# Kernel tuning notes

Measured on AMD Instinct MI355X. Metric: run time of the kernel, lower is better.

The kernel has to match this reference:

```python
import jax, jax.numpy as jnp
import numpy as np

# RReLU in eval mode is leaky_relu with slope = (lower+upper)/2 = (1/8 + 1/3)/2
RRELU_SLOPE = (1.0 / 8.0 + 1.0 / 3.0) / 2.0  # = 11/48

N_NODES, FEAT_DIM = 100000, 512
EMBED_DIM = 256
BATCH, NUM_SAMPLE = 16384, 10


def setup_inputs() -> dict:
    key = jax.random.key(0)
    k1, k2, k3 = jax.random.split(key, 3)
    features = jax.random.normal(k1, (N_NODES, FEAT_DIM), dtype=jnp.float32)
    # Xavier-uniform-style init for the weight [embed_dim, feat_dim]
    bound = float(np.sqrt(6.0 / (EMBED_DIM + FEAT_DIM)))
    weight = jax.random.uniform(k2, (EMBED_DIM, FEAT_DIM), dtype=jnp.float32,
                                minval=-bound, maxval=bound)
    # Pre-sampled neighbor ids per batch node: [BATCH, NUM_SAMPLE]
    neigh_idx = jax.random.randint(k3, (BATCH, NUM_SAMPLE), 0, N_NODES, dtype=jnp.int64)
    return {"features": features, "weight": weight, "neigh_idx": neigh_idx}


def reference(features, weight, neigh_idx):
    # Mean aggregator: gather sampled neighbor features and average -> [B, F]
    agg = jnp.take(features, neigh_idx, axis=0).mean(axis=1)
    # weight.mm(agg.t()) -> [E, B]
    y = jnp.einsum("ef,bf->eb", weight, agg)
    # RReLU (eval mode): leaky with mean slope
    return jnp.where(y >= 0, y, y * RRELU_SLOPE)
```

## Files before the change

### kernel.cpp

```cpp
#include <hip/hip_runtime.h>
#include <stdint.h>

constexpr int FEAT  = 512;
constexpr int EMB   = 256;
constexpr int BATCH = 16384;
constexpr int NSAMP = 10;
constexpr int NB    = 64;
constexpr float SLOPE  = 11.0f / 48.0f;
constexpr float INV_NS = 1.0f / 10.0f;

using f32x4 = __attribute__((ext_vector_type(4))) float;
using frag8 = __attribute__((ext_vector_type(8))) short;

static __device__ __forceinline__ unsigned f2b(float x) {
    unsigned u = __builtin_bit_cast(unsigned, x);
    return (u + 0x7fffu + ((u >> 16) & 1u)) >> 16;
}
static __device__ __forceinline__ unsigned pk2(float lo, float hi) {
    return f2b(lo) | (f2b(hi) << 16);
}

__global__ __launch_bounds__(512, 2) void enc_fused(const float* __restrict__ feat,
                                                    const float* __restrict__ wgt,
                                                    const int*   __restrict__ idx,
                                                    float*       __restrict__ out) {
    __shared__ ushort Bs[NB * FEAT];

    const int tid  = threadIdx.x;
    const int wv   = tid >> 6;
    const int lane = tid & 63;
    const int n0   = blockIdx.x * NB;

#pragma unroll 2
    for (int rr = 0; rr < 8; ++rr) {
        const int r  = wv * 8 + rr;
        const int ru = __builtin_amdgcn_readfirstlane(r);
        const int* ib = idx + (size_t)(n0 + ru) * NSAMP;
        f32x4 s0 = {0.f, 0.f, 0.f, 0.f}, s1 = {0.f, 0.f, 0.f, 0.f};
#pragma unroll
        for (int j = 0; j < NSAMP; ++j) {
            const float* fp = feat + (size_t)ib[j] * FEAT + lane * 8;
            const f32x4 v0 = *reinterpret_cast<const f32x4*>(fp);
            const f32x4 v1 = *reinterpret_cast<const f32x4*>(fp + 4);
            s0 += v0; s1 += v1;
        }
        union { frag8 f; unsigned u[4]; } o;
        o.u[0] = pk2(s0[0] * INV_NS, s0[1] * INV_NS);
        o.u[1] = pk2(s0[2] * INV_NS, s0[3] * INV_NS);
        o.u[2] = pk2(s1[0] * INV_NS, s1[1] * INV_NS);
        o.u[3] = pk2(s1[2] * INV_NS, s1[3] * INV_NS);
        const int kb = (lane * 16) ^ ((r & 7) << 4);
        *reinterpret_cast<frag8*>((char*)Bs + r * (FEAT * 2) + kb) = o.f;
    }
    __syncthreads();

    const int l15 = lane & 15, lq = lane >> 4;
    const int m0w = wv * 32;

    f32x4 acc[2][4] = {};

#pragma unroll
    for (int k0 = 0; k0 < FEAT; k0 += 32) {
        frag8 af[2], bf[4];
#pragma unroll
        for (int i = 0; i < 2; ++i) {
            const float* wp = wgt + (size_t)(m0w + i * 16 + l15) * FEAT + k0 + lq * 8;
            const f32x4 a0 = *reinterpret_cast<const f32x4*>(wp);
            const f32x4 a1 = *reinterpret_cast<const f32x4*>(wp + 4);
            union { frag8 f; unsigned u[4]; } pk;
            pk.u[0] = pk2(a0[0], a0[1]);
            pk.u[1] = pk2(a0[2], a0[3]);
            pk.u[2] = pk2(a1[0], a1[1]);
            pk.u[3] = pk2(a1[2], a1[3]);
            af[i] = pk.f;
        }
#pragma unroll
        for (int j = 0; j < 4; ++j) {
            const int row = j * 16 + l15;
            const int kb  = (k0 * 2 + lq * 16) ^ ((row & 7) << 4);
            bf[j] = *reinterpret_cast<const frag8*>((const char*)Bs + row * (FEAT * 2) + kb);
        }
#pragma unroll
        for (int i = 0; i < 2; ++i)
#pragma unroll
            for (int j = 0; j < 4; ++j)
                acc[i][j] = __builtin_amdgcn_mfma_f32_16x16x32_bf16(af[i], bf[j], acc[i][j], 0, 0, 0);
    }

#pragma unroll
    for (int i = 0; i < 2; ++i) {
        const int rb = m0w + i * 16 + lq * 4;
#pragma unroll
        for (int j = 0; j < 4; ++j) {
            const int col = n0 + j * 16 + l15;
#pragma unroll
            for (int q = 0; q < 4; ++q) {
                float y = acc[i][j][q];
                y = (y >= 0.f) ? y : y * SLOPE;
                out[(size_t)(rb + q) * BATCH + col] = y;
            }
        }
    }
}

extern "C" void kernel_launch(void* const* d_in, const int* in_sizes, int n_in,
                              void* d_out, int out_size, void* d_ws, size_t ws_size,
                              hipStream_t stream) {
    const float* feat = (const float*)d_in[0];
    const float* wgt  = (const float*)d_in[1];
    const int*   idx  = (const int*)d_in[2];
    float*       out  = (float*)d_out;

    enc_fused<<<BATCH / NB, 512, 0, stream>>>(feat, wgt, idx, out);
}
```

Measured before the change: 68.19 us.

## Use 1024-thread blocks with 16 waves, each owning a 16-row output strip

```diff
diff --git a/kernel.cpp b/kernel.cpp
--- a/kernel.cpp
+++ b/kernel.cpp
@@ -1,4 +1,5 @@
 #include <hip/hip_runtime.h>
+#include <hip/hip_bf16.h>
 #include <stdint.h>
 
 constexpr int FEAT  = 512;
@@ -6,24 +7,24 @@
 constexpr int BATCH = 16384;
 constexpr int NSAMP = 10;
 constexpr int NB    = 64;
+constexpr int NW    = 16;
+constexpr int RPW   = NB / NW;
 constexpr float SLOPE  = 11.0f / 48.0f;
 constexpr float INV_NS = 1.0f / 10.0f;
 
 using f32x4 = __attribute__((ext_vector_type(4))) float;
 using frag8 = __attribute__((ext_vector_type(8))) short;
 
-static __device__ __forceinline__ unsigned f2b(float x) {
-    unsigned u = __builtin_bit_cast(unsigned, x);
-    return (u + 0x7fffu + ((u >> 16) & 1u)) >> 16;
-}
-static __device__ __forceinline__ unsigned pk2(float lo, float hi) {
-    return f2b(lo) | (f2b(hi) << 16);
+static __device__ __forceinline__ unsigned bpack2(float a, float b) {
+    __hip_bfloat162 h = __float22bfloat162_rn(make_float2(a, b));
+    unsigned u; __builtin_memcpy(&u, &h, 4);
+    return u;
 }
 
-__global__ __launch_bounds__(512, 2) void enc_fused(const float* __restrict__ feat,
-                                                    const float* __restrict__ wgt,
-                                                    const int*   __restrict__ idx,
-                                                    float*       __restrict__ out) {
+__global__ __launch_bounds__(1024, 4) void enc_fused(const float* __restrict__ feat,
+                                                     const float* __restrict__ wgt,
+                                                     const int*   __restrict__ idx,
+                                                     float*       __restrict__ out) {
     __shared__ ushort Bs[NB * FEAT];
 
     const int tid  = threadIdx.x;
@@ -32,8 +33,8 @@
     const int n0   = blockIdx.x * NB;
 
 #pragma unroll 2
-    for (int rr = 0; rr < 8; ++rr) {
-        const int r  = wv * 8 + rr;
+    for (int rr = 0; rr < RPW; ++rr) {
+        const int r  = wv * RPW + rr;
         const int ru = __builtin_amdgcn_readfirstlane(r);
         const int* ib = idx + (size_t)(n0 + ru) * NSAMP;
         f32x4 s0 = {0.f, 0.f, 0.f, 0.f}, s1 = {0.f, 0.f, 0.f, 0.f};
@@ -45,60 +46,52 @@
             s0 += v0; s1 += v1;
         }
         union { frag8 f; unsigned u[4]; } o;
-        o.u[0] = pk2(s0[0] * INV_NS, s0[1] * INV_NS);
-        o.u[1] = pk2(s0[2] * INV_NS, s0[3] * INV_NS);
-        o.u[2] = pk2(s1[0] * INV_NS, s1[1] * INV_NS);
-        o.u[3] = pk2(s1[2] * INV_NS, s1[3] * INV_NS);
+        o.u[0] = bpack2(s0[0] * INV_NS, s0[1] * INV_NS);
+        o.u[1] = bpack2(s0[2] * INV_NS, s0[3] * INV_NS);
+        o.u[2] = bpack2(s1[0] * INV_NS, s1[1] * INV_NS);
+        o.u[3] = bpack2(s1[2] * INV_NS, s1[3] * INV_NS);
         const int kb = (lane * 16) ^ ((r & 7) << 4);
         *reinterpret_cast<frag8*>((char*)Bs + r * (FEAT * 2) + kb) = o.f;
     }
     __syncthreads();
 
     const int l15 = lane & 15, lq = lane >> 4;
-    const int m0w = wv * 32;
+    const int m0w = wv * 16;
 
-    f32x4 acc[2][4] = {};
+    f32x4 acc[4] = {};
 
 #pragma unroll
     for (int k0 = 0; k0 < FEAT; k0 += 32) {
-        frag8 af[2], bf[4];
-#pragma unroll
-        for (int i = 0; i < 2; ++i) {
-            const float* wp = wgt + (size_t)(m0w + i * 16 + l15) * FEAT + k0 + lq * 8;
+        frag8 af, bf[4];
+        {
+            const float* wp = wgt + (size_t)(m0w + l15) * FEAT + k0 + lq * 8;
             const f32x4 a0 = *reinterpret_cast<const f32x4*>(wp);
             const f32x4 a1 = *reinterpret_cast<const f32x4*>(wp + 4);
-            union { frag8 f; unsigned u[4]; } pk;
-            pk.u[0] = pk2(a0[0], a0[1]);
-            pk.u[1] = pk2(a0[2], a0[3]);
-            pk.u[2] = pk2(a1[0], a1[1]);
-            pk.u[3] = pk2(a1[2], a1[3]);
-            af[i] = pk.f;
+            union { unsigned u[4]; frag8 f; } pk;
+            pk.u[0] = bpack2(a0[0], a0[1]); pk.u[1] = bpack2(a0[2], a0[3]);
+            pk.u[2] = bpack2(a1[0], a1[1]); pk.u[3] = bpack2(a1[2], a1[3]);
+            af = pk.f;
         }
 #pragma unroll
-        for (int j = 0; j < 4; ++j) {
-            const int row = j * 16 + l15;
+        for (int jj = 0; jj < 4; ++jj) {
+            const int row = jj * 16 + l15;
             const int kb  = (k0 * 2 + lq * 16) ^ ((row & 7) << 4);
-            bf[j] = *reinterpret_cast<const frag8*>((const char*)Bs + row * (FEAT * 2) + kb);
+            bf[jj] = *reinterpret_cast<const frag8*>((const char*)Bs + row * (FEAT * 2) + kb);
         }
 #pragma unroll
-        for (int i = 0; i < 2; ++i)
-#pragma unroll
-            for (int j = 0; j < 4; ++j)
-                acc[i][j] = __builtin_amdgcn_mfma_f32_16x16x32_bf16(af[i], bf[j], acc[i][j], 0, 0, 0);
+        for (int jj = 0; jj < 4; ++jj)
+            acc[jj] = __builtin_amdgcn_mfma_f32_16x16x32_bf16(af, bf[jj], acc[jj], 0, 0, 0);
     }
 
 #pragma unroll
-    for (int i = 0; i < 2; ++i) {
-        const int rb = m0w + i * 16 + lq * 4;
+    for (int jj = 0; jj < 4; ++jj) {
+        const int col = n0 + jj * 16 + l15;
 #pragma unroll
-        for (int j = 0; j < 4; ++j) {
-            const int col = n0 + j * 16 + l15;
-#pragma unroll
-            for (int q = 0; q < 4; ++q) {
-                float y = acc[i][j][q];
-                y = (y >= 0.f) ? y : y * SLOPE;
-                out[(size_t)(rb + q) * BATCH + col] = y;
-            }
+        for (int q = 0; q < 4; ++q) {
+            const int row = m0w + lq * 4 + q;
+            float y = acc[jj][q];
+            y = (y >= 0.f) ? y : y * SLOPE;
+            out[(size_t)row * BATCH + col] = y;
         }
     }
 }
@@ -111,5 +104,5 @@
     const int*   idx  = (const int*)d_in[2];
     float*       out  = (float*)d_out;
 
-    enc_fused<<<BATCH / NB, 512, 0, stream>>>(feat, wgt, idx, out);
+    enc_fused<<<BATCH / NB, 1024, 0, stream>>>(feat, wgt, idx, out);
 }
```

Result: no change. 67.16 us (-1.5%).
